# Performance work log

Hardware: AMD Instinct MI355X
Metric: run time of the kernel (lower is better)

The kernel has to match this reference:

```python
import jax, jax.numpy as jnp
import numpy as np

NUM_EXPERTS = 8
TOP_K = 2
D_MODEL = 1024
D_FF = 4096
TOKENS = 8192


def setup_inputs() -> dict:
    key = jax.random.key(0)
    ks = jax.random.split(key, 7)
    s_in = 1.0 / np.sqrt(D_MODEL)
    s_ff = 1.0 / np.sqrt(D_FF)
    return {
        "x": jax.random.normal(ks[0], (TOKENS, D_MODEL), dtype=jnp.float32),
        "gate_w": jax.random.normal(ks[1], (D_MODEL, NUM_EXPERTS), dtype=jnp.float32) * s_in,
        "gate_b": jnp.zeros((NUM_EXPERTS,), dtype=jnp.float32),
        "w1": jax.random.normal(ks[2], (NUM_EXPERTS, D_MODEL, D_FF), dtype=jnp.float32) * s_in,
        "b1": jnp.zeros((NUM_EXPERTS, D_FF), dtype=jnp.float32),
        "w2": jax.random.normal(ks[3], (NUM_EXPERTS, D_FF, D_MODEL), dtype=jnp.float32) * s_ff,
        "b2": jnp.zeros((NUM_EXPERTS, D_MODEL), dtype=jnp.float32),
    }


def reference(x, gate_w, gate_b, w1, b1, w2, b2):
    # gate: softmax over experts, then top-k routing
    probs = jax.nn.softmax(x @ gate_w + gate_b, axis=-1)  # [T, E]
    topk_p, topk_i = jax.lax.top_k(probs, TOP_K)          # [T, K]
    T, E = probs.shape
    # dense per-token combine weights: zero for unrouted experts
    comb = jnp.zeros((T, E), dtype=x.dtype).at[jnp.arange(T)[:, None], topk_i].set(topk_p)
    out = jnp.zeros_like(x)
    for e in range(E):  # small fixed expert loop; math identical to masked gather/scatter
        h = jax.nn.silu(x @ w1[e] + b1[e])                # [T, D_FF]
        out = out + comb[:, e:e + 1] * (h @ w2[e] + b2[e])
    return out
```

## Files before the change

kernel.cpp:

```cpp
#include <hip/hip_runtime.h>
#include <hip/hip_bf16.h>
#include <math.h>

#define TOKENS 8192
#define DMODEL 1024
#define DFF    4096
#define NEXP   8
#define PAD_H     17664
#define ESTRIDE   8448
#define MAX_SLOTS 72
#define BK 64

typedef __bf16 bf16;
typedef bf16  bf16x4 __attribute__((ext_vector_type(4)));
typedef bf16  bf16x8 __attribute__((ext_vector_type(8)));
typedef float f32x4  __attribute__((ext_vector_type(4)));

__device__ __forceinline__ void gload16(const bf16* g, bf16* l) {
    __builtin_amdgcn_global_load_lds(
        (const __attribute__((address_space(1))) void*)g,
        (__attribute__((address_space(3))) void*)l,
        16, 0, 0);
}

__global__ __launch_bounds__(256) void gate_kernel(
    const float* __restrict__ x, const float* __restrict__ gw, const float* __restrict__ gb,
    int* __restrict__ cursor, int* __restrict__ token_ids, float* __restrict__ pair_p,
    bf16* __restrict__ xb)
{
    int wid  = (blockIdx.x * blockDim.x + threadIdx.x) >> 6;
    int lane = threadIdx.x & 63;
    if (wid >= TOKENS) return;
    const float* xr = x + (size_t)wid * DMODEL;
    bf16* xbr = xb + (size_t)wid * DMODEL;
    float a0=0,a1=0,a2=0,a3=0,a4=0,a5=0,a6=0,a7=0;
    #pragma unroll
    for (int i = 0; i < 4; ++i) {
        int cq = i*256 + lane*4;
        float4 xv = *(const float4*)(xr + cq);
        bf16x4 xc = { (bf16)xv.x, (bf16)xv.y, (bf16)xv.z, (bf16)xv.w };
        *(bf16x4*)(xbr + cq) = xc;
        #pragma unroll
        for (int j = 0; j < 4; ++j) {
            float xe = (j==0)?xv.x:(j==1)?xv.y:(j==2)?xv.z:xv.w;
            const float4* g = (const float4*)(gw + (size_t)(cq + j) * NEXP);
            float4 g0 = g[0], g1 = g[1];
            a0 += xe * g0.x; a1 += xe * g0.y; a2 += xe * g0.z; a3 += xe * g0.w;
            a4 += xe * g1.x; a5 += xe * g1.y; a6 += xe * g1.z; a7 += xe * g1.w;
        }
    }
    #pragma unroll
    for (int off = 32; off; off >>= 1) {
        a0 += __shfl_xor(a0, off); a1 += __shfl_xor(a1, off);
        a2 += __shfl_xor(a2, off); a3 += __shfl_xor(a3, off);
        a4 += __shfl_xor(a4, off); a5 += __shfl_xor(a5, off);
        a6 += __shfl_xor(a6, off); a7 += __shfl_xor(a7, off);
    }
    if (lane == 0) {
        float l[NEXP] = { a0+gb[0], a1+gb[1], a2+gb[2], a3+gb[3],
                          a4+gb[4], a5+gb[5], a6+gb[6], a7+gb[7] };
        float m = l[0];
        #pragma unroll
        for (int e = 1; e < NEXP; ++e) m = fmaxf(m, l[e]);
        float p[NEXP], s = 0.f;
        #pragma unroll
        for (int e = 0; e < NEXP; ++e) { p[e] = expf(l[e] - m); s += p[e]; }
        float inv = 1.0f / s;
        int i1 = 0; float b1v = p[0];
        #pragma unroll
        for (int e = 1; e < NEXP; ++e) if (p[e] > b1v) { b1v = p[e]; i1 = e; }
        int i2 = -1; float b2v = -1.f;
        #pragma unroll
        for (int e = 0; e < NEXP; ++e) if (e != i1 && p[e] > b2v) { b2v = p[e]; i2 = e; }
        int idx1 = atomicAdd(&cursor[i1], 1);
        int idx2 = atomicAdd(&cursor[i2], 1);
        token_ids[i1*ESTRIDE + idx1] = wid;
        pair_p   [i1*ESTRIDE + idx1] = b1v * inv;
        token_ids[i2*ESTRIDE + idx2] = wid | 0x2000;
        pair_p   [i2*ESTRIDE + idx2] = b2v * inv;
    }
}

__global__ void build_slots(const int* __restrict__ counts, int* n_slots,
                            int* slot_e, int* slot_row0, int* slot_gbase)
{
    __shared__ int sc[8], spb[9], stb[9];
    int t = threadIdx.x;
    if (t < 8) sc[t] = counts[t];
    __syncthreads();
    if (t == 0) {
        int pb = 0, tb = 0;
        for (int e = 0; e < NEXP; ++e) {
            spb[e] = pb; stb[e] = tb;
            pb += ((sc[e] + 127) >> 7) << 7;
            tb += (sc[e] + 255) >> 8;
        }
        spb[8] = pb; stb[8] = tb;
        *n_slots = tb;
    }
    __syncthreads();
    if (t < stb[8]) { int e = 0; while (t >= stb[e+1]) ++e;
        slot_e[t] = e; slot_row0[t] = (t - stb[e]) << 8; slot_gbase[t] = spb[e]; }
}

__global__ __launch_bounds__(256) void transpose_cvt(
    const float* __restrict__ src, bf16* __restrict__ dst, int R, int C)
{
    __shared__ bf16 tile[64 * 72];
    int e = blockIdx.z;
    int c0 = blockIdx.x * 64, r0 = blockIdx.y * 64;
    const float* s = src + (size_t)e * R * C;
    bf16* d = dst + (size_t)e * R * C;
    int t = threadIdx.x;
    {
        int r = t >> 2, q = t & 3;
        const float4* sp = (const float4*)(s + (size_t)(r0 + r) * C + c0 + q * 16);
        float4 v0 = sp[0], v1 = sp[1], v2 = sp[2], v3 = sp[3];
        bf16x8 p0, p1;
        p0[0]=(bf16)v0.x; p0[1]=(bf16)v0.y; p0[2]=(bf16)v0.z; p0[3]=(bf16)v0.w;
        p0[4]=(bf16)v1.x; p0[5]=(bf16)v1.y; p0[6]=(bf16)v1.z; p0[7]=(bf16)v1.w;
        p1[0]=(bf16)v2.x; p1[1]=(bf16)v2.y; p1[2]=(bf16)v2.z; p1[3]=(bf16)v2.w;
        p1[4]=(bf16)v3.x; p1[5]=(bf16)v3.y; p1[6]=(bf16)v3.z; p1[7]=(bf16)v3.w;
        bf16* w = tile + r * 72 + (q ^ (r >> 4)) * 16;
        *(bf16x8*)w = p0; *(bf16x8*)(w + 8) = p1;
    }
    __syncthreads();
    {
        int c = t >> 2, rq = t & 3;
        int gc = c >> 4, cl = c & 15;
        bf16x8 q0, q1;
        #pragma unroll
        for (int k = 0; k < 8; ++k) {
            q0[k] = tile[(rq*16 + k) * 72 + (gc ^ rq) * 16 + cl];
            q1[k] = tile[(rq*16 + 8 + k) * 72 + (gc ^ rq) * 16 + cl];
        }
        bf16* dp = d + (size_t)(c0 + c) * R + r0 + rq * 16;
        *(bf16x8*)dp = q0;
        *(bf16x8*)(dp + 8) = q1;
    }
}

__global__ __launch_bounds__(512, 2) void moe_gemm1(
    const bf16* __restrict__ Xb, const bf16* __restrict__ Bt,
    const float* __restrict__ bias, bf16* __restrict__ Hout,
    const int* __restrict__ token_ids,
    const int* __restrict__ slot_e, const int* __restrict__ slot_row0,
    const int* __restrict__ slot_gbase, const int* __restrict__ n_slots,
    const int* __restrict__ counts)
{
    constexpr int K = DMODEL, N = DFF, NJT = N / 256, NT = K / BK, NITER = NT / 2;

    int nwg = gridDim.x, bid = blockIdx.x;
    int wid = (bid & 7) * (nwg >> 3) + (bid >> 3);
    int slot = wid / NJT;
    if (slot >= *n_slots) return;
    int jt = wid % NJT;
    int e = slot_e[slot], row0 = slot_row0[slot], gbase = slot_gbase[slot];
    int cnt = counts[e];
    int pad_e = (cnt + 127) & ~127;
    int tlb = e * ESTRIDE;

    __shared__ __align__(16) bf16 shm[65536];

    int t = threadIdx.x, lane = t & 63, wv = t >> 6;
    int wm = wv >> 2, wn = wv & 3;
    int lr = lane & 15, kq = lane >> 4;
    int bh = wn >> 1, bro = (wn & 1) * 64;

    int aoff[2][2]; int boff[2][2];
    const bf16* Bbase = Bt + (size_t)e * N * K;
    int g8 = ((lane & 7) ^ (lane >> 3)) * 8;
    #pragma unroll
    for (int h = 0; h < 2; ++h)
        #pragma unroll
        for (int q = 0; q < 2; ++q) {
            int rloc = h*128 + wv*16 + q*8 + (lane >> 3);
            int tok = token_ids[tlb + row0 + rloc] & 0x1FFF;
            aoff[h][q] = tok * DMODEL + g8;
            boff[h][q] = (jt*256 + rloc) * K + g8;
        }

    f32x4 acc[8][4] = {};
    bf16x8 breg[4][2];

    #define STAGE_A(S, H, T) do { int _t = ((T) < NT ? (T) : 0) * BK;                   \
        gload16(Xb + aoff[H][0] + _t, shm + (((S)*2+(H))*128 + wv*16    ) * BK);        \
        gload16(Xb + aoff[H][1] + _t, shm + (((S)*2+(H))*128 + wv*16 + 8) * BK); } while(0)
    #define STAGE_B(S, H, T) do { int _t = ((T) < NT ? (T) : 0) * BK;                           \
        gload16(Bbase + boff[H][0] + _t, shm + 32768 + (((S)*2+(H))*128 + wv*16    ) * BK);     \
        gload16(Bbase + boff[H][1] + _t, shm + 32768 + (((S)*2+(H))*128 + wv*16 + 8) * BK); } while(0)

    STAGE_A(0,0,0); STAGE_A(0,1,0); STAGE_B(0,0,0); STAGE_B(0,1,0);
    STAGE_B(1,0,1); STAGE_B(1,1,1);
    asm volatile("s_waitcnt vmcnt(4)" ::: "memory");
    __builtin_amdgcn_s_barrier();

    #define LOAD_A(S, Q)                                                             \
        _Pragma("unroll") for (int mi = 0; mi < 2; ++mi)                             \
            _Pragma("unroll") for (int kk = 0; kk < 2; ++kk)                         \
                areg[mi][kk] = *(const bf16x8*)(shm +                                \
                    (((S)*2+wm)*128 + ((Q)*2+mi)*16 + lr) * BK +                     \
                    ((kk*4+kq) ^ (lr & 7)) * 8);
    #define MFMA_Q(Q)                                                                \
        __builtin_amdgcn_s_setprio(1);                                               \
        _Pragma("unroll") for (int mi = 0; mi < 2; ++mi)                             \
            _Pragma("unroll") for (int n = 0; n < 4; ++n)                            \
                _Pragma("unroll") for (int kk = 0; kk < 2; ++kk)                     \
                    acc[(Q)*2+mi][n] = __builtin_amdgcn_mfma_f32_16x16x32_bf16(      \
                        areg[mi][kk], breg[n][kk], acc[(Q)*2+mi][n], 0, 0, 0);       \
        __builtin_amdgcn_s_setprio(0);

    #define PHASE2(S, Q2, STAGE_CODE, DO_WAIT)                                       \
    {                                                                                \
        bf16x8 areg[2][2];                                                           \
        if ((Q2) == 0) {                                                             \
            _Pragma("unroll") for (int n = 0; n < 4; ++n)                            \
                _Pragma("unroll") for (int kk = 0; kk < 2; ++kk)                     \
                    breg[n][kk] = *(const bf16x8*)(shm + 32768 +                     \
                        (((S)*2+bh)*128 + bro + n*16 + lr) * BK +                    \
                        ((kk*4+kq) ^ (lr & 7)) * 8);                                 \
        }                                                                            \
        LOAD_A(S, (Q2)*2)                                                            \
        STAGE_CODE;                                                                  \
        asm volatile("" ::: "memory");                                               \
        __builtin_amdgcn_s_barrier();                                                \
        MFMA_Q((Q2)*2)                                                               \
        LOAD_A(S, (Q2)*2+1)                                                          \
        MFMA_Q((Q2)*2+1)                                                             \
        if (DO_WAIT) asm volatile("s_waitcnt vmcnt(4)" ::: "memory");                \
        asm volatile("" ::: "memory");                                               \
        __builtin_amdgcn_s_barrier();                                                \
    }

    for (int i = 0; i < NITER; ++i) {
        int TO = 2*i+1, TE2 = 2*i+2, TO2 = 2*i+3;
        PHASE2(0, 0, { STAGE_A(1,0,TO);  STAGE_A(1,1,TO);  }, 0)
        PHASE2(0, 1, { STAGE_B(0,0,TE2); STAGE_B(0,1,TE2); }, 1)
        PHASE2(1, 0, { STAGE_A(0,0,TE2); STAGE_A(0,1,TE2); }, 0)
        PHASE2(1, 1, { STAGE_B(1,0,TO2); STAGE_B(1,1,TO2); }, 1)
    }
    asm volatile("s_waitcnt vmcnt(0)" ::: "memory");
    #undef PHASE2
    #undef MFMA_Q
    #undef LOAD_A
    #undef STAGE_A
    #undef STAGE_B

    int lro = kq * 4;
    float bv[4];
    #pragma unroll
    for (int n = 0; n < 4; ++n)
        bv[n] = bias[e * DFF + jt*256 + wn*64 + n*16 + lr];
    #pragma unroll
    for (int m = 0; m < 8; ++m)
        #pragma unroll
        for (int reg = 0; reg < 4; ++reg) {
            int rl = wm*128 + m*16 + lro + reg;
            if (row0 + rl < pad_e) {
                size_t hrow = (size_t)(gbase + row0 + rl);
                #pragma unroll
                for (int n = 0; n < 4; ++n) {
                    int col = jt*256 + wn*64 + n*16 + lr;
                    float v = acc[m][n][reg] + bv[n];
                    v = v / (1.0f + __expf(-v));
                    __builtin_nontemporal_store((bf16)v, &Hout[hrow * DFF + col]);
                }
            }
        }
}

__global__ __launch_bounds__(512, 2) void moe_gemm2(
    const bf16* __restrict__ Ah, const bf16* __restrict__ Bt,
    const float* __restrict__ bias, float* __restrict__ pbuf,
    const int* __restrict__ token_ids, const float* __restrict__ pair_p,
    const int* __restrict__ slot_e, const int* __restrict__ slot_row0,
    const int* __restrict__ slot_gbase, const int* __restrict__ n_slots,
    const int* __restrict__ counts)
{
    constexpr int K = DFF, N = DMODEL, NJT = N / 128, NT = K / BK;

    int nwg = gridDim.x, bid = blockIdx.x;
    int wid = (bid & 7) * (nwg >> 3) + (bid >> 3);
    int slot = wid / NJT;
    if (slot >= *n_slots) return;
    int jt = wid % NJT;
    int e = slot_e[slot], row0 = slot_row0[slot], gbase = slot_gbase[slot];
    int cnt = counts[e];
    int tlb = e * ESTRIDE;

    __shared__ __align__(16) bf16 shm[49152];

    int t = threadIdx.x, lane = t & 63, wv = t >> 6;
    int wm4 = wv >> 1, wn2 = wv & 1;
    int lr = lane & 15, kq = lane >> 4;
    int g8 = ((lane & 7) ^ (lane >> 3)) * 8;

    int aoff[4], boff[2];
    const bf16* Bbase = Bt + (size_t)e * N * K;
    #pragma unroll
    for (int q = 0; q < 4; ++q) {
        int rloc = wv*32 + q*8 + (lane >> 3);
        aoff[q] = (gbase + row0 + rloc) * DFF + g8;
    }
    #pragma unroll
    for (int q = 0; q < 2; ++q) {
        int rloc = wv*16 + q*8 + (lane >> 3);
        boff[q] = (jt*128 + rloc) * K + g8;
    }

    f32x4 acc[4][4] = {};

    #define ST2(S, T) do { int _t = ((T) < NT ? (T) : 0) * BK;                        \
        _Pragma("unroll") for (int q = 0; q < 4; ++q)                                 \
            gload16(Ah + aoff[q] + _t, shm + (S)*16384 + (wv*32 + q*8)*BK);           \
        _Pragma("unroll") for (int q = 0; q < 2; ++q)                                 \
            gload16(Bbase + boff[q] + _t, shm + 32768 + (S)*8192 + (wv*16 + q*8)*BK); \
        } while (0)

    ST2(0, 0);
    for (int tt = 0; tt < NT; ++tt) {
        int c = tt & 1;
        ST2(c ^ 1, tt + 1);
        asm volatile("s_waitcnt vmcnt(6)" ::: "memory");
        __builtin_amdgcn_s_barrier();
        bf16x8 areg[4][2], breg[4][2];
        #pragma unroll
        for (int m = 0; m < 4; ++m)
            #pragma unroll
            for (int kk = 0; kk < 2; ++kk)
                areg[m][kk] = *(const bf16x8*)(shm + c*16384 +
                    (wm4*64 + m*16 + lr)*BK + ((kk*4+kq) ^ (lr & 7))*8);
        #pragma unroll
        for (int n = 0; n < 4; ++n)
            #pragma unroll
            for (int kk = 0; kk < 2; ++kk)
                breg[n][kk] = *(const bf16x8*)(shm + 32768 + c*8192 +
                    (wn2*64 + n*16 + lr)*BK + ((kk*4+kq) ^ (lr & 7))*8);
        __builtin_amdgcn_s_setprio(1);
        #pragma unroll
        for (int m = 0; m < 4; ++m)
            #pragma unroll
            for (int n = 0; n < 4; ++n)
                #pragma unroll
                for (int kk = 0; kk < 2; ++kk)
                    acc[m][n] = __builtin_amdgcn_mfma_f32_16x16x32_bf16(
                        areg[m][kk], breg[n][kk], acc[m][n], 0, 0, 0);
        __builtin_amdgcn_s_setprio(0);
        asm volatile("" ::: "memory");
        __builtin_amdgcn_s_barrier();
    }
    asm volatile("s_waitcnt vmcnt(0)" ::: "memory");
    #undef ST2

    float bv[4];
    #pragma unroll
    for (int n = 0; n < 4; ++n)
        bv[n] = bias[e * DMODEL + jt*128 + wn2*64 + n*16 + lr];
    #pragma unroll
    for (int m = 0; m < 4; ++m)
        #pragma unroll
        for (int reg = 0; reg < 4; ++reg) {
            int rl = wm4*64 + m*16 + kq*4 + reg;
            if (row0 + rl < cnt) {
                int pr = tlb + row0 + rl;
                int tw = token_ids[pr];
                int tok = tw & 0x1FFF, wh = (tw >> 13) & 1;
                float p = pair_p[pr];
                float* dst = pbuf + ((size_t)(tok*2 + wh)) * DMODEL;
                #pragma unroll
                for (int n = 0; n < 4; ++n) {
                    int col = jt*128 + wn2*64 + n*16 + lr;
                    __builtin_nontemporal_store(p * (acc[m][n][reg] + bv[n]), &dst[col]);
                }
            }
        }
}

__global__ __launch_bounds__(256) void combine_kernel(
    const float* __restrict__ pbuf, float* __restrict__ out)
{
    int wid  = (blockIdx.x * 256 + threadIdx.x) >> 6;
    int lane = threadIdx.x & 63;
    const f32x4* a = (const f32x4*)(pbuf + (size_t)wid * 2 * DMODEL);
    const f32x4* b = (const f32x4*)(pbuf + ((size_t)wid * 2 + 1) * DMODEL);
    f32x4* o = (f32x4*)(out + (size_t)wid * DMODEL);
    #pragma unroll
    for (int i = 0; i < 4; ++i) {
        int c = i*64 + lane;
        o[c] = a[c] + b[c];
    }
}

extern "C" void kernel_launch(void* const* d_in, const int* in_sizes, int n_in,
                              void* d_out, int out_size, void* d_ws, size_t ws_size,
                              hipStream_t stream)
{
    const float* x  = (const float*)d_in[0];
    const float* gw = (const float*)d_in[1];
    const float* gb = (const float*)d_in[2];
    const float* w1 = (const float*)d_in[3];
    const float* b1 = (const float*)d_in[4];
    const float* w2 = (const float*)d_in[5];
    const float* b2 = (const float*)d_in[6];
    float* out = (float*)d_out;

    const size_t W1T_OFF = 0;
    const size_t W2T_OFF = 67108864;
    const size_t H_OFF   = 134217728;
    const size_t S_OFF   = H_OFF + (size_t)17408 * DFF * 2;
    const size_t WS_NEEDED = S_OFF + 4096 + 2 * (NEXP * ESTRIDE * 4);
    if (ws_size < WS_NEEDED) return;

    char* ws = (char*)d_ws;
    bf16*  w1t  = (bf16*)(ws + W1T_OFF);
    float* pbuf = (float*)(ws + W1T_OFF);
    bf16*  w2t  = (bf16*)(ws + W2T_OFF);
    bf16*  xb   = (bf16*)(ws + W2T_OFF);
    bf16*  h    = (bf16*)(ws + H_OFF);
    char*  S    = ws + S_OFF;
    int*   cursor    = (int*)(S + 0);
    int*   n_slots   = (int*)(S + 64);
    int*   slot_e    = (int*)(S + 128);
    int*   slot_row0 = (int*)(S + 512);
    int*   slot_gbase= (int*)(S + 896);
    int*   token_ids = (int*)(S + 4096);
    float* pair_p    = (float*)(S + 4096 + NEXP * ESTRIDE * 4);

    hipMemsetAsync(cursor, 0, 64, stream);

    transpose_cvt<<<dim3(DFF/64, DMODEL/64, NEXP), dim3(256), 0, stream>>>(w1, w1t, DMODEL, DFF);

    gate_kernel<<<TOKENS * 64 / 256, 256, 0, stream>>>(x, gw, gb, cursor, token_ids, pair_p, xb);
    build_slots<<<1, 128, 0, stream>>>(cursor, n_slots, slot_e, slot_row0, slot_gbase);

    moe_gemm1<<<MAX_SLOTS * (DFF/256), 512, 0, stream>>>(
        xb, w1t, b1, h, token_ids, slot_e, slot_row0, slot_gbase, n_slots, cursor);

    transpose_cvt<<<dim3(DMODEL/64, DFF/64, NEXP), dim3(256), 0, stream>>>(w2, w2t, DFF, DMODEL);

    moe_gemm2<<<MAX_SLOTS * (DMODEL/128), 512, 0, stream>>>(
        h, w2t, b2, pbuf, token_ids, pair_p, slot_e, slot_row0, slot_gbase, n_slots, cursor);

    combine_kernel<<<TOKENS * 64 / 256, 256, 0, stream>>>(pbuf, out);
}
```

Baseline: 694.6 us.

## Deterministic ballot-based expert compaction and triple-buffered loads in second GEMM

```diff
diff --git a/kernel.cpp b/kernel.cpp
--- a/kernel.cpp
+++ b/kernel.cpp
@@ -6,7 +6,6 @@
 #define DMODEL 1024
 #define DFF    4096
 #define NEXP   8
-#define PAD_H     17664
 #define ESTRIDE   8448
 #define MAX_SLOTS 72
 #define BK 64
@@ -25,8 +24,7 @@
 
 __global__ __launch_bounds__(256) void gate_kernel(
     const float* __restrict__ x, const float* __restrict__ gw, const float* __restrict__ gb,
-    int* __restrict__ cursor, int* __restrict__ token_ids, float* __restrict__ pair_p,
-    bf16* __restrict__ xb)
+    int2* __restrict__ topk_i, float2* __restrict__ topk_p, bf16* __restrict__ xb)
 {
     int wid  = (blockIdx.x * blockDim.x + threadIdx.x) >> 6;
     int lane = threadIdx.x & 63;
@@ -72,13 +70,33 @@
         int i2 = -1; float b2v = -1.f;
         #pragma unroll
         for (int e = 0; e < NEXP; ++e) if (e != i1 && p[e] > b2v) { b2v = p[e]; i2 = e; }
-        int idx1 = atomicAdd(&cursor[i1], 1);
-        int idx2 = atomicAdd(&cursor[i2], 1);
-        token_ids[i1*ESTRIDE + idx1] = wid;
-        pair_p   [i1*ESTRIDE + idx1] = b1v * inv;
-        token_ids[i2*ESTRIDE + idx2] = wid | 0x2000;
-        pair_p   [i2*ESTRIDE + idx2] = b2v * inv;
-    }
+        topk_i[wid] = make_int2(i1, i2);
+        topk_p[wid] = make_float2(b1v * inv, b2v * inv);
+    }
+}
+
+__global__ __launch_bounds__(64) void compact_kernel(
+    const int2* __restrict__ topk_i, const float2* __restrict__ topk_p,
+    int* __restrict__ counts, int* __restrict__ token_ids, float* __restrict__ pair_p)
+{
+    int e = blockIdx.x;
+    int lane = threadIdx.x;
+    int base = 0;
+    for (int it = 0; it < TOKENS/64; ++it) {
+        int t = it*64 + lane;
+        int2 ki = topk_i[t];
+        bool hit = (ki.x == e) || (ki.y == e);
+        int which = (ki.y == e) ? 1 : 0;
+        unsigned long long m = __ballot(hit);
+        if (hit) {
+            int idx = base + __popcll(m & ((1ull << lane) - 1ull));
+            float2 kp = topk_p[t];
+            token_ids[e*ESTRIDE + idx] = t | (which << 13);
+            pair_p   [e*ESTRIDE + idx] = which ? kp.y : kp.x;
+        }
+        base += __popcll(m);
+    }
+    if (lane == 0) counts[e] = base;
 }
 
 __global__ void build_slots(const int* __restrict__ counts, int* n_slots,
@@ -288,7 +306,7 @@
     int cnt = counts[e];
     int tlb = e * ESTRIDE;
 
-    __shared__ __align__(16) bf16 shm[49152];
+    __shared__ __align__(16) bf16 shm[73728];
 
     int t = threadIdx.x, lane = t & 63, wv = t >> 6;
     int wm4 = wv >> 1, wn2 = wv & 1;
@@ -314,27 +332,27 @@
         _Pragma("unroll") for (int q = 0; q < 4; ++q)                                 \
             gload16(Ah + aoff[q] + _t, shm + (S)*16384 + (wv*32 + q*8)*BK);           \
         _Pragma("unroll") for (int q = 0; q < 2; ++q)                                 \
-            gload16(Bbase + boff[q] + _t, shm + 32768 + (S)*8192 + (wv*16 + q*8)*BK); \
+            gload16(Bbase + boff[q] + _t, shm + 49152 + (S)*8192 + (wv*16 + q*8)*BK); \
         } while (0)
 
-    ST2(0, 0);
+    ST2(0, 0); ST2(1, 1);
+    int cs = 0, ps = 2;
     for (int tt = 0; tt < NT; ++tt) {
-        int c = tt & 1;
-        ST2(c ^ 1, tt + 1);
-        asm volatile("s_waitcnt vmcnt(6)" ::: "memory");
+        ST2(ps, tt + 2);
+        asm volatile("s_waitcnt vmcnt(12)" ::: "memory");
         __builtin_amdgcn_s_barrier();
         bf16x8 areg[4][2], breg[4][2];
         #pragma unroll
         for (int m = 0; m < 4; ++m)
             #pragma unroll
             for (int kk = 0; kk < 2; ++kk)
-                areg[m][kk] = *(const bf16x8*)(shm + c*16384 +
+                areg[m][kk] = *(const bf16x8*)(shm + cs*16384 +
                     (wm4*64 + m*16 + lr)*BK + ((kk*4+kq) ^ (lr & 7))*8);
         #pragma unroll
         for (int n = 0; n < 4; ++n)
             #pragma unroll
             for (int kk = 0; kk < 2; ++kk)
-                breg[n][kk] = *(const bf16x8*)(shm + 32768 + c*8192 +
+                breg[n][kk] = *(const bf16x8*)(shm + 49152 + cs*8192 +
                     (wn2*64 + n*16 + lr)*BK + ((kk*4+kq) ^ (lr & 7))*8);
         __builtin_amdgcn_s_setprio(1);
         #pragma unroll
@@ -348,6 +366,8 @@
         __builtin_amdgcn_s_setprio(0);
         asm volatile("" ::: "memory");
         __builtin_amdgcn_s_barrier();
+        cs = (cs == 2) ? 0 : cs + 1;
+        ps = (ps == 2) ? 0 : ps + 1;
     }
     asm volatile("s_waitcnt vmcnt(0)" ::: "memory");
     #undef ST2
@@ -408,7 +428,7 @@
     const size_t W2T_OFF = 67108864;
     const size_t H_OFF   = 134217728;
     const size_t S_OFF   = H_OFF + (size_t)17408 * DFF * 2;
-    const size_t WS_NEEDED = S_OFF + 4096 + 2 * (NEXP * ESTRIDE * 4);
+    const size_t WS_NEEDED = S_OFF + 4096 + 2*(NEXP*ESTRIDE*4) + 2*(TOKENS*8);
     if (ws_size < WS_NEEDED) return;
 
     char* ws = (char*)d_ws;
@@ -418,28 +438,29 @@
     bf16*  xb   = (bf16*)(ws + W2T_OFF);
     bf16*  h    = (bf16*)(ws + H_OFF);
     char*  S    = ws + S_OFF;
-    int*   cursor    = (int*)(S + 0);
+    int*   counts    = (int*)(S + 0);
     int*   n_slots   = (int*)(S + 64);
     int*   slot_e    = (int*)(S + 128);
     int*   slot_row0 = (int*)(S + 512);
     int*   slot_gbase= (int*)(S + 896);
     int*   token_ids = (int*)(S + 4096);
-    float* pair_p    = (float*)(S + 4096 + NEXP * ESTRIDE * 4);
-
-    hipMemsetAsync(cursor, 0, 64, stream);
+    float* pair_p    = (float*)(S + 4096 + NEXP*ESTRIDE*4);
+    int2*  topk_i    = (int2*)(S + 4096 + 2*(NEXP*ESTRIDE*4));
+    float2* topk_p   = (float2*)(S + 4096 + 2*(NEXP*ESTRIDE*4) + TOKENS*8);
 
     transpose_cvt<<<dim3(DFF/64, DMODEL/64, NEXP), dim3(256), 0, stream>>>(w1, w1t, DMODEL, DFF);
 
-    gate_kernel<<<TOKENS * 64 / 256, 256, 0, stream>>>(x, gw, gb, cursor, token_ids, pair_p, xb);
-    build_slots<<<1, 128, 0, stream>>>(cursor, n_slots, slot_e, slot_row0, slot_gbase);
+    gate_kernel<<<TOKENS * 64 / 256, 256, 0, stream>>>(x, gw, gb, topk_i, topk_p, xb);
+    compact_kernel<<<NEXP, 64, 0, stream>>>(topk_i, topk_p, counts, token_ids, pair_p);
+    build_slots<<<1, 128, 0, stream>>>(counts, n_slots, slot_e, slot_row0, slot_gbase);
 
     moe_gemm1<<<MAX_SLOTS * (DFF/256), 512, 0, stream>>>(
-        xb, w1t, b1, h, token_ids, slot_e, slot_row0, slot_gbase, n_slots, cursor);
+        xb, w1t, b1, h, token_ids, slot_e, slot_row0, slot_gbase, n_slots, counts);
 
     transpose_cvt<<<dim3(DMODEL/64, DFF/64, NEXP), dim3(256), 0, stream>>>(w2, w2t, DFF, DMODEL);
 
     moe_gemm2<<<MAX_SLOTS * (DMODEL/128), 512, 0, stream>>>(
-        h, w2t, b2, pbuf, token_ids, pair_p, slot_e, slot_row0, slot_gbase, n_slots, cursor);
+        h, w2t, b2, pbuf, token_ids, pair_p, slot_e, slot_row0, slot_gbase, n_slots, counts);
 
     combine_kernel<<<TOKENS * 64 / 256, 256, 0, stream>>>(pbuf, out);
 }
```

New measurement: 591.7 us. -14.8%, faster.
